# Kernel tuning notes

Hardware: AMD Instinct MI355X
Metric: run time of the kernel (lower is better)

The kernel has to match this reference:

```python
import jax, jax.numpy as jnp
import numpy as np
from math import sqrt

P = 1.0  # axis-aligned transform exponent (init arg p)
EPS = 1e-6


def setup_inputs() -> dict:
    key = jax.random.key(0)
    k1, k2, k3, k4 = jax.random.split(key, 4)
    B, L, S, H, E = 4, 2048, 2048, 8, 64
    return {
        "queries": jax.random.normal(k1, (B, L, H, E), dtype=jnp.float32),
        "keys": jax.random.normal(k2, (B, S, H, E), dtype=jnp.float32),
        "values": jax.random.normal(k3, (B, S, H, E), dtype=jnp.float32),
        "attn_mask": jnp.zeros((1, 1, 1, 1), dtype=bool),  # unused: mask_flag=False
        "directional_weights": jnp.ones((1, 1, 1, 1), dtype=jnp.float32),
        "dynamic_param": jax.random.normal(k4, (1,), dtype=jnp.float32),
    }


def _transform(x, directional_weights, dynamic_param):
    # axis_aligned_transformation: rescale by (1/std over seq dim)^p (unbiased std, like torch)
    std = jnp.std(x, axis=-2, keepdims=True, ddof=1)
    x = x * (1.0 / (std + EPS)) ** P
    # directional_reweighting then nonlinear_mapping
    x = x * directional_weights
    return jnp.tanh(x) * dynamic_param


def reference(queries, keys, values, attn_mask, directional_weights, dynamic_param):
    B, L, H, E = queries.shape
    scale = 1.0 / sqrt(E)
    qt = _transform(queries, directional_weights, dynamic_param)  # [B,L,H,E]
    kt = _transform(keys, directional_weights, dynamic_param)     # [B,S,H,E]
    scores = jnp.einsum('blhe,bshe->bhls', qt, kt)                # [B,H,L,S]
    # per-row tau = sqrt(var(scores) + eps), unbiased variance like torch.var
    tau = jnp.sqrt(jnp.var(scores, axis=-1, keepdims=True, ddof=1) + EPS)
    A = jax.nn.softmax(scale * scores / tau, axis=-1)             # [B,H,L,S]
    V = jnp.einsum('bhls,bshd->blhd', A, values)                  # [B,L,H,D]
    return V
```

## Files before the change

kernel.cpp:

```cpp
#include <hip/hip_runtime.h>
#include <math.h>

#define B_ 4
#define L_ 2048
#define S_ 2048
#define H_ 8
#define E_ 64
#define BH_ (B_*H_)
#define EPS 1e-6f
#define LOG2E 1.44269504088896340736f

typedef __attribute__((ext_vector_type(8))) short short8;
typedef __attribute__((ext_vector_type(4))) float f32x4;

__device__ __forceinline__ unsigned short f2bf(float f) {
    unsigned int u = __float_as_uint(f);
    u = (u + 0x7fffu + ((u >> 16) & 1u)) >> 16;
    return (unsigned short)u;
}

__device__ __forceinline__ float bf2f(unsigned short u) {
    return __uint_as_float(((unsigned int)u) << 16);
}

__device__ __forceinline__ float fast_tanh(float x) {
    float e = __expf(2.0f * x);
    return 1.0f - 2.0f / (e + 1.0f);
}

__device__ __forceinline__ unsigned int cvt_pk_bf16(float lo, float hi) {
    unsigned int r;
    asm("v_cvt_pk_bf16_f32 %0, %1, %2" : "=v"(r) : "v"(lo), "v"(hi));
    return r;
}
__device__ __forceinline__ float exp2_fast(float x) {
    float r;
    asm("v_exp_f32 %0, %1" : "=v"(r) : "v"(x));
    return r;
}
__device__ __forceinline__ void swap32(unsigned int &a, unsigned int &b) {
    asm("v_permlane32_swap_b32 %0, %1" : "+v"(a), "+v"(b));
}
__device__ __forceinline__ void swap16(unsigned int &a, unsigned int &b) {
    asm("v_permlane16_swap_b32 %0, %1" : "+v"(a), "+v"(b));
}

__global__ __launch_bounds__(256) void pre_kernel(
    const float* __restrict__ xq, const float* __restrict__ xk,
    const float* __restrict__ xv,
    unsigned short* __restrict__ qt, unsigned short* __restrict__ kt,
    unsigned short* __restrict__ vt,
    const float* __restrict__ dwp, const float* __restrict__ dpp)
{
    __shared__ float ls[64][65];
    int bx = blockIdx.x;
    int tid = threadIdx.x;
    if (bx < 4096) {
        const float* x = (bx < 2048) ? xq : xk;
        unsigned short* xt = (bx < 2048) ? qt : kt;
        int wv = tid >> 6, ln = tid & 63;
        int bl = (bx & 2047) * 4 + wv;
        int b = bl >> 11, l = bl & 2047;
        const float* xb = x + (size_t)bl * 512;
        float4 fa = *(const float4*)(xb + ln * 4);
        float4 fb = *(const float4*)(xb + 256 + ln * 4);
        float s0 = fa.x + fb.x, s1 = fa.y + fb.y, s2 = fa.z + fb.z, s3 = fa.w + fb.w;
        float q0 = fa.x * fa.x + fb.x * fb.x, q1 = fa.y * fa.y + fb.y * fb.y;
        float q2 = fa.z * fa.z + fb.z * fb.z, q3 = fa.w * fa.w + fb.w * fb.w;
        s0 += __shfl_xor(s0, 16); s1 += __shfl_xor(s1, 16);
        s2 += __shfl_xor(s2, 16); s3 += __shfl_xor(s3, 16);
        q0 += __shfl_xor(q0, 16); q1 += __shfl_xor(q1, 16);
        q2 += __shfl_xor(q2, 16); q3 += __shfl_xor(q3, 16);
        s0 += __shfl_xor(s0, 32); s1 += __shfl_xor(s1, 32);
        s2 += __shfl_xor(s2, 32); s3 += __shfl_xor(s3, 32);
        q0 += __shfl_xor(q0, 32); q1 += __shfl_xor(q1, 32);
        q2 += __shfl_xor(q2, 32); q3 += __shfl_xor(q3, 32);
        float dw = dwp[0], d = dpp[0];
        auto mkw = [&](float s, float q) {
            float mean = s * 0.125f;
            float var = (q - s * mean) * (1.f / 7.f);
            var = fmaxf(var, 0.f);
            return dw / (sqrtf(var) + EPS);
        };
        float w0 = mkw(s0, q0), w1 = mkw(s1, q1), w2 = mkw(s2, q2), w3 = mkw(s3, q3);
        float ta0 = fast_tanh(fa.x * w0) * d, ta1 = fast_tanh(fa.y * w1) * d;
        float ta2 = fast_tanh(fa.z * w2) * d, ta3 = fast_tanh(fa.w * w3) * d;
        float tb0 = fast_tanh(fb.x * w0) * d, tb1 = fast_tanh(fb.y * w1) * d;
        float tb2 = fast_tanh(fb.z * w2) * d, tb3 = fast_tanh(fb.w * w3) * d;
        uint2 pa, pb;
        pa.x = cvt_pk_bf16(ta0, ta1); pa.y = cvt_pk_bf16(ta2, ta3);
        pb.x = cvt_pk_bf16(tb0, tb1); pb.y = cvt_pk_bf16(tb2, tb3);
        int hh = ln >> 4, e0 = (ln & 15) * 4;
        *(uint2*)(xt + ((size_t)(b * 8 + hh) * 2048 + l) * 64 + e0) = pa;
        *(uint2*)(xt + ((size_t)(b * 8 + hh + 4) * 2048 + l) * 64 + e0) = pb;
    } else {
        int t2 = bx - 4096;
        int s0 = (t2 & 31) * 64;
        int h = (t2 >> 5) & 7, b = t2 >> 8;
        int t = tid;
#pragma unroll
        for (int i = 0; i < 4; ++i) {
            int idx = t + i * 256;
            int r = idx >> 4, c4 = (idx & 15) * 4;
            const float4 f = *(const float4*)&xv[((size_t)(b * S_ + s0 + r) * H_ + h) * E_ + c4];
            ls[r][c4] = f.x; ls[r][c4 + 1] = f.y; ls[r][c4 + 2] = f.z; ls[r][c4 + 3] = f.w;
        }
        __syncthreads();
        size_t ob = ((size_t)(b * H_ + h) * (S_ / 64) + (s0 >> 6)) * 4096;
#pragma unroll
        for (int i = 0; i < 2; ++i) {
            int ri = t + i * 256;
            int et = ri >> 7, c = (ri >> 6) & 1, quad = (ri >> 4) & 3, m = ri & 15;
            int e = et * 16 + m, sb = c * 32 + quad * 8;
            unsigned short tmp[8];
#pragma unroll
            for (int j = 0; j < 8; ++j) tmp[j] = f2bf(ls[sb + j][e]);
            *(uint4*)&vt[ob + (size_t)ri * 8] = *(uint4*)tmp;
        }
    }
}

__global__ __launch_bounds__(256) void gram_kernel(
    unsigned short* __restrict__ kt, unsigned short* __restrict__ Gb,
    float* __restrict__ ksum)
{
    __shared__ unsigned short ks[128 * 72];
    __shared__ float gs[4096];
    __shared__ float kss[64];
    int bh = blockIdx.x;
    unsigned short* base = kt + (size_t)bh * S_ * E_;
    int tid = threadIdx.x, lane = tid & 63, w = tid >> 6;
    int m = lane & 15, quad = lane >> 4;

    f32x4 acc[4][4];
#pragma unroll
    for (int i = 0; i < 4; ++i)
#pragma unroll
        for (int j = 0; j < 4; ++j) acc[i][j] = (f32x4){0.f, 0.f, 0.f, 0.f};
    float ksp[4] = {0.f, 0.f, 0.f, 0.f};

    short8 stg[4];
#pragma unroll
    for (int i = 0; i < 4; ++i)
        stg[i] = *(const short8*)(base + (size_t)(tid + i * 256) * 8);

    for (int ch = 0; ch < 16; ++ch) {
        __syncthreads();
#pragma unroll
        for (int i = 0; i < 4; ++i) {
            int u = tid + i * 256;
            *(short8*)&ks[(u >> 3) * 72 + (u & 7) * 8] = stg[i];
        }
        __syncthreads();
        if (ch < 15) {
#pragma unroll
            for (int i = 0; i < 4; ++i)
                stg[i] = *(const short8*)(base + (size_t)(ch + 1) * 8192 + (tid + i * 256) * 8);
        }
#pragma unroll
        for (int tt = 0; tt < 2; ++tt)
#pragma unroll
            for (int i = 0; i < 2; ++i) {
                int u = tid + i * 256;
                int nt = u >> 7, cc = (u >> 6) & 1, ln2 = u & 63;
                int mm = ln2 & 15, qq = ln2 >> 4;
                short8 vv = *(const short8*)&ks[(tt * 64 + nt * 16 + mm) * 72 + cc * 32 + qq * 8];
                *(uint4*)&base[(size_t)(ch * 2 + tt) * 4096 + (size_t)u * 8] = *(uint4*)&vv;
            }
        int s0 = w * 32;
        short8 af[4];
#pragma unroll
        for (int i = 0; i < 4; ++i) {
            short8 a;
#pragma unroll
            for (int kk = 0; kk < 8; ++kk) {
                unsigned short uv = ks[(s0 + quad * 8 + kk) * 72 + i * 16 + m];
                a[kk] = (short)uv;
                ksp[i] += bf2f(uv);
            }
            af[i] = a;
        }
#pragma unroll
        for (int i = 0; i < 4; ++i)
#pragma unroll
            for (int j = 0; j < 4; ++j)
                acc[i][j] = __builtin_amdgcn_mfma_f32_16x16x32_bf16(af[i], af[j], acc[i][j], 0, 0, 0);
    }
#pragma unroll
    for (int i = 0; i < 4; ++i) {
        ksp[i] += __shfl_xor(ksp[i], 16);
        ksp[i] += __shfl_xor(ksp[i], 32);
    }
    for (int w2 = 0; w2 < 4; ++w2) {
        if (w == w2) {
#pragma unroll
            for (int i = 0; i < 4; ++i)
#pragma unroll
                for (int j = 0; j < 4; ++j)
#pragma unroll
                    for (int r = 0; r < 4; ++r) {
                        int idx = (i * 16 + quad * 4 + r) * 64 + j * 16 + m;
                        if (w2 == 0) gs[idx] = acc[i][j][r]; else gs[idx] += acc[i][j][r];
                    }
            if (lane < 16) {
#pragma unroll
                for (int i = 0; i < 4; ++i) {
                    int e = i * 16 + lane;
                    if (w2 == 0) kss[e] = ksp[i]; else kss[e] += ksp[i];
                }
            }
        }
        __syncthreads();
    }
#pragma unroll
    for (int ii = 0; ii < 16; ++ii) {
        int idx = tid + ii * 256;
        Gb[(size_t)bh * 4096 + idx] = f2bf(gs[idx]);
    }
    if (tid < 64) ksum[bh * 64 + tid] = kss[tid];
}

__global__ __launch_bounds__(256, 2) void attn_kernel(
    const unsigned short* __restrict__ qt,
    const unsigned short* __restrict__ ktf,
    const unsigned short* __restrict__ vt,
    const unsigned short* __restrict__ Gb,
    const float* __restrict__ ksum,
    float* __restrict__ out)
{
    __shared__ float2 ascr_s[4 * 32];
    const int tid = threadIdx.x;
    const int lane = tid & 63;
    const int w = tid >> 6;
    const int m = lane & 15;
    const int quad = lane >> 4;
    float2* ascr = ascr_s + w * 32;

    int blk = blockIdx.x;
    int bh = (blk & 7) * 4 + ((blk >> 3) & 3);
    int l0 = (blk >> 5) * 128;
    int b = bh >> 3, h = bh & 7;

    const unsigned short* qtb = qt + (size_t)bh * L_ * E_;
    const unsigned short* kb  = ktf + (size_t)bh * S_ * E_;
    const unsigned short* vtb = vt + (size_t)bh * (S_ / 64) * 4096;

    short8 qf[2][2];
#pragma unroll
    for (int g = 0; g < 2; ++g)
#pragma unroll
        for (int c = 0; c < 2; ++c)
            qf[g][c] = *(const short8*)(qtb + (size_t)(l0 + w * 32 + g * 16 + m) * E_ + c * 32 + quad * 8);

    float al2[2], nalm2[2];
    {
        const unsigned short* gb = Gb + (size_t)bh * 4096;
        short8 gfr[4][2];
#pragma unroll
        for (int j = 0; j < 4; ++j)
#pragma unroll
            for (int c = 0; c < 2; ++c)
                gfr[j][c] = *(const short8*)(gb + (size_t)(j * 16 + m) * 64 + c * 32 + quad * 8);
        float ksl[4];
#pragma unroll
        for (int j = 0; j < 4; ++j) ksl[j] = ksum[bh * 64 + j * 16 + m];
#pragma unroll
        for (int g = 0; g < 2; ++g) {
            f32x4 accj[4];
#pragma unroll
            for (int j = 0; j < 4; ++j) {
                accj[j] = (f32x4){0.f, 0.f, 0.f, 0.f};
                accj[j] = __builtin_amdgcn_mfma_f32_16x16x32_bf16(qf[g][0], gfr[j][0], accj[j], 0, 0, 0);
                accj[j] = __builtin_amdgcn_mfma_f32_16x16x32_bf16(qf[g][1], gfr[j][1], accj[j], 0, 0, 0);
            }
            float ps[4] = {0, 0, 0, 0}, pr[4] = {0, 0, 0, 0};
#pragma unroll
            for (int r = 0; r < 4; ++r)
#pragma unroll
                for (int j = 0; j < 4; ++j) {
                    float qv = bf2f(qtb[(size_t)(l0 + w * 32 + g * 16 + quad * 4 + r) * E_ + j * 16 + m]);
                    ps[r] = fmaf(accj[j][r], qv, ps[r]);
                    pr[r] = fmaf(qv, ksl[j], pr[r]);
                }
#pragma unroll
            for (int mask = 1; mask < 16; mask <<= 1)
#pragma unroll
                for (int r = 0; r < 4; ++r) {
                    ps[r] += __shfl_xor(ps[r], mask);
                    pr[r] += __shfl_xor(pr[r], mask);
                }
            if (m == 0) {
#pragma unroll
                for (int r = 0; r < 4; ++r) {
                    float sum = pr[r];
                    float mu = sum * (1.f / S_);
                    float var = (ps[r] - sum * mu) * (1.f / (S_ - 1));
                    var = fmaxf(var, 0.f);
                    float tau = sqrtf(var + EPS);
                    float a = 0.125f / tau;
                    ascr[g * 16 + quad * 4 + r] = make_float2(a, a * mu);
                }
            }
        }
#pragma unroll
        for (int g = 0; g < 2; ++g) {
            float2 a2 = ascr[g * 16 + m];
            al2[g] = a2.x * LOG2E; nalm2[g] = -a2.y * LOG2E;
        }
    }

    f32x4 oacc[2][4];
#pragma unroll
    for (int g = 0; g < 2; ++g)
#pragma unroll
        for (int et = 0; et < 4; ++et) oacc[g][et] = (f32x4){0.f, 0.f, 0.f, 0.f};
    f32x4 asum2[2];
#pragma unroll
    for (int g = 0; g < 2; ++g) asum2[g] = (f32x4){0.f, 0.f, 0.f, 0.f};

    short8 ones;
#pragma unroll
    for (int j = 0; j < 8; ++j) ones[j] = (short)0x3F80;

#pragma unroll 2
    for (int st = 0; st < S_ / 64; ++st) {
        const unsigned short* kstb = kb + (size_t)st * 4096;
        const unsigned short* vstb = vtb + (size_t)st * 4096;
        short8 kf[4][2];
#pragma unroll
        for (int nt = 0; nt < 4; ++nt)
#pragma unroll
            for (int c = 0; c < 2; ++c)
                kf[nt][c] = *(const short8*)(kstb + (nt * 2 + c) * 512 + lane * 8);
        short8 vf[2][4];
#pragma unroll
        for (int c = 0; c < 2; ++c)
#pragma unroll
            for (int et = 0; et < 4; ++et)
                vf[c][et] = *(const short8*)(vstb + et * 1024 + c * 512 + lane * 8);

        unsigned int W[2][4][2];
#pragma unroll
        for (int nt = 0; nt < 4; ++nt)
#pragma unroll
            for (int g = 0; g < 2; ++g) {
                f32x4 acc = (f32x4){0.f, 0.f, 0.f, 0.f};
                acc = __builtin_amdgcn_mfma_f32_16x16x32_bf16(kf[nt][0], qf[g][0], acc, 0, 0, 0);
                acc = __builtin_amdgcn_mfma_f32_16x16x32_bf16(kf[nt][1], qf[g][1], acc, 0, 0, 0);
                float p0 = exp2_fast(fmaf(al2[g], acc[0], nalm2[g]));
                float p1 = exp2_fast(fmaf(al2[g], acc[1], nalm2[g]));
                float p2 = exp2_fast(fmaf(al2[g], acc[2], nalm2[g]));
                float p3 = exp2_fast(fmaf(al2[g], acc[3], nalm2[g]));
                W[g][nt][0] = cvt_pk_bf16(p0, p1);
                W[g][nt][1] = cvt_pk_bf16(p2, p3);
            }
#pragma unroll
        for (int g = 0; g < 2; ++g) {
            short8 pf[2];
#pragma unroll
            for (int c = 0; c < 2; ++c) {
                unsigned int a0 = W[g][2 * c][0], b0 = W[g][2 * c + 1][0];
                unsigned int a1 = W[g][2 * c][1], b1 = W[g][2 * c + 1][1];
                swap32(a0, b0); swap16(a0, b0);
                swap32(a1, b1); swap16(a1, b1);
                uint4 pk4;
                pk4.x = a0; pk4.y = a1; pk4.z = b0; pk4.w = b1;
                pf[c] = *(short8*)&pk4;
            }
#pragma unroll
            for (int et = 0; et < 4; ++et) {
                oacc[g][et] = __builtin_amdgcn_mfma_f32_16x16x32_bf16(pf[0], vf[0][et], oacc[g][et], 0, 0, 0);
                oacc[g][et] = __builtin_amdgcn_mfma_f32_16x16x32_bf16(pf[1], vf[1][et], oacc[g][et], 0, 0, 0);
            }
            asum2[g] = __builtin_amdgcn_mfma_f32_16x16x32_bf16(pf[0], ones, asum2[g], 0, 0, 0);
            asum2[g] = __builtin_amdgcn_mfma_f32_16x16x32_bf16(pf[1], ones, asum2[g], 0, 0, 0);
        }
    }

#pragma unroll
    for (int g = 0; g < 2; ++g)
#pragma unroll
        for (int r = 0; r < 4; ++r) {
            float rd = 1.0f / asum2[g][r];
            size_t row = (size_t)(b * L_ + l0 + w * 32 + g * 16 + quad * 4 + r);
#pragma unroll
            for (int et = 0; et < 4; ++et)
                out[(row * H_ + h) * E_ + et * 16 + m] = oacc[g][et][r] * rd;
        }
}

extern "C" void kernel_launch(void* const* d_in, const int* in_sizes, int n_in,
                              void* d_out, int out_size, void* d_ws, size_t ws_size,
                              hipStream_t stream)
{
    const float* q = (const float*)d_in[0];
    const float* k = (const float*)d_in[1];
    const float* v = (const float*)d_in[2];
    const float* dw = (const float*)d_in[4];
    const float* dp = (const float*)d_in[5];
    float* out = (float*)d_out;

    unsigned short* qt = (unsigned short*)d_ws;
    unsigned short* kt = qt + (size_t)BH_ * L_ * E_;
    unsigned short* vt = kt + (size_t)BH_ * S_ * E_;
    unsigned short* Gb = vt + (size_t)BH_ * E_ * S_;
    float* ksum = (float*)(Gb + (size_t)BH_ * 4096);

    pre_kernel<<<5120, 256, 0, stream>>>(q, k, v, qt, kt, vt, dw, dp);
    gram_kernel<<<BH_, 256, 0, stream>>>(kt, Gb, ksum);
    attn_kernel<<<512, 256, 0, stream>>>(qt, kt, vt, Gb, ksum, out);
}
```

Measured before the change: 163.4 us.

## Split Gram reduction across four blocks per head with fp32 atomics

The Gram/key-sum kernel now launches four blocks per batch-head, each covering a quarter of the sequence, instead of one block per head. Partial results are accumulated with atomicAdd into an fp32 buffer that extra blocks in the preprocessing kernel zero out first. The attention kernel converts this fp32 Gram matrix to bf16 when it loads it. This targets the low occupancy of a 32-block launch on a GPU with many CUs, at the cost of atomic traffic and a separate zeroing pass. The attention kernel also raises wave priority around its PV MFMA block.

After: 157.9 us. 3.3% less time.

```diff
diff --git a/kernel.cpp b/kernel.cpp
--- a/kernel.cpp
+++ b/kernel.cpp
@@ -49,7 +49,7 @@
     const float* __restrict__ xq, const float* __restrict__ xk,
     const float* __restrict__ xv,
     unsigned short* __restrict__ qt, unsigned short* __restrict__ kt,
-    unsigned short* __restrict__ vt,
+    unsigned short* __restrict__ vt, float* __restrict__ Gf,
     const float* __restrict__ dwp, const float* __restrict__ dpp)
 {
     __shared__ float ls[64][65];
@@ -93,7 +93,7 @@
         int hh = ln >> 4, e0 = (ln & 15) * 4;
         *(uint2*)(xt + ((size_t)(b * 8 + hh) * 2048 + l) * 64 + e0) = pa;
         *(uint2*)(xt + ((size_t)(b * 8 + hh + 4) * 2048 + l) * 64 + e0) = pb;
-    } else {
+    } else if (bx < 5120) {
         int t2 = bx - 4096;
         int s0 = (t2 & 31) * 64;
         int h = (t2 >> 5) & 7, b = t2 >> 8;
@@ -117,18 +117,21 @@
             for (int j = 0; j < 8; ++j) tmp[j] = f2bf(ls[sb + j][e]);
             *(uint4*)&vt[ob + (size_t)ri * 8] = *(uint4*)tmp;
         }
+    } else {
+        for (int i = (bx - 5120) * 256 + tid; i < 32 * 4096 + 32 * 64; i += 32 * 256)
+            Gf[i] = 0.f;
     }
 }
 
 __global__ __launch_bounds__(256) void gram_kernel(
-    unsigned short* __restrict__ kt, unsigned short* __restrict__ Gb,
+    unsigned short* __restrict__ kt, float* __restrict__ Gf,
     float* __restrict__ ksum)
 {
     __shared__ unsigned short ks[128 * 72];
     __shared__ float gs[4096];
-    __shared__ float kss[64];
-    int bh = blockIdx.x;
-    unsigned short* base = kt + (size_t)bh * S_ * E_;
+    int g2 = blockIdx.x;
+    int bh = g2 >> 2, part = g2 & 3;
+    unsigned short* base = kt + (size_t)bh * S_ * E_ + (size_t)part * 512 * E_;
     int tid = threadIdx.x, lane = tid & 63, w = tid >> 6;
     int m = lane & 15, quad = lane >> 4;
 
@@ -144,7 +147,7 @@
     for (int i = 0; i < 4; ++i)
         stg[i] = *(const short8*)(base + (size_t)(tid + i * 256) * 8);
 
-    for (int ch = 0; ch < 16; ++ch) {
+    for (int ch = 0; ch < 4; ++ch) {
         __syncthreads();
 #pragma unroll
         for (int i = 0; i < 4; ++i) {
@@ -152,7 +155,7 @@
             *(short8*)&ks[(u >> 3) * 72 + (u & 7) * 8] = stg[i];
         }
         __syncthreads();
-        if (ch < 15) {
+        if (ch < 3) {
 #pragma unroll
             for (int i = 0; i < 4; ++i)
                 stg[i] = *(const short8*)(base + (size_t)(ch + 1) * 8192 + (tid + i * 256) * 8);
@@ -191,6 +194,11 @@
         ksp[i] += __shfl_xor(ksp[i], 16);
         ksp[i] += __shfl_xor(ksp[i], 32);
     }
+    if (lane < 16) {
+#pragma unroll
+        for (int i = 0; i < 4; ++i)
+            atomicAdd(&ksum[bh * 64 + i * 16 + lane], ksp[i]);
+    }
     for (int w2 = 0; w2 < 4; ++w2) {
         if (w == w2) {
 #pragma unroll
@@ -202,29 +210,21 @@
                         int idx = (i * 16 + quad * 4 + r) * 64 + j * 16 + m;
                         if (w2 == 0) gs[idx] = acc[i][j][r]; else gs[idx] += acc[i][j][r];
                     }
-            if (lane < 16) {
-#pragma unroll
-                for (int i = 0; i < 4; ++i) {
-                    int e = i * 16 + lane;
-                    if (w2 == 0) kss[e] = ksp[i]; else kss[e] += ksp[i];
-                }
-            }
         }
         __syncthreads();
     }
 #pragma unroll
     for (int ii = 0; ii < 16; ++ii) {
         int idx = tid + ii * 256;
-        Gb[(size_t)bh * 4096 + idx] = f2bf(gs[idx]);
-    }
-    if (tid < 64) ksum[bh * 64 + tid] = kss[tid];
+        atomicAdd(&Gf[bh * 4096 + idx], gs[idx]);
+    }
 }
 
 __global__ __launch_bounds__(256, 2) void attn_kernel(
     const unsigned short* __restrict__ qt,
     const unsigned short* __restrict__ ktf,
     const unsigned short* __restrict__ vt,
-    const unsigned short* __restrict__ Gb,
+    const float* __restrict__ Gf,
     const float* __restrict__ ksum,
     float* __restrict__ out)
 {
@@ -254,13 +254,20 @@
 
     float al2[2], nalm2[2];
     {
-        const unsigned short* gb = Gb + (size_t)bh * 4096;
+        const float* gb = Gf + (size_t)bh * 4096;
         short8 gfr[4][2];
 #pragma unroll
         for (int j = 0; j < 4; ++j)
 #pragma unroll
-            for (int c = 0; c < 2; ++c)
-                gfr[j][c] = *(const short8*)(gb + (size_t)(j * 16 + m) * 64 + c * 32 + quad * 8);
+            for (int c = 0; c < 2; ++c) {
+                const float* gp = gb + (size_t)(j * 16 + m) * 64 + c * 32 + quad * 8;
+                float4 f0 = *(const float4*)gp;
+                float4 f1 = *(const float4*)(gp + 4);
+                uint4 u;
+                u.x = cvt_pk_bf16(f0.x, f0.y); u.y = cvt_pk_bf16(f0.z, f0.w);
+                u.z = cvt_pk_bf16(f1.x, f1.y); u.w = cvt_pk_bf16(f1.z, f1.w);
+                gfr[j][c] = *(short8*)&u;
+            }
         float ksl[4];
 #pragma unroll
         for (int j = 0; j < 4; ++j) ksl[j] = ksum[bh * 64 + j * 16 + m];
@@ -367,6 +374,7 @@
                 pk4.x = a0; pk4.y = a1; pk4.z = b0; pk4.w = b1;
                 pf[c] = *(short8*)&pk4;
             }
+            __builtin_amdgcn_s_setprio(1);
 #pragma unroll
             for (int et = 0; et < 4; ++et) {
                 oacc[g][et] = __builtin_amdgcn_mfma_f32_16x16x32_bf16(pf[0], vf[0][et], oacc[g][et], 0, 0, 0);
@@ -374,6 +382,7 @@
             }
             asum2[g] = __builtin_amdgcn_mfma_f32_16x16x32_bf16(pf[0], ones, asum2[g], 0, 0, 0);
             asum2[g] = __builtin_amdgcn_mfma_f32_16x16x32_bf16(pf[1], ones, asum2[g], 0, 0, 0);
+            __builtin_amdgcn_s_setprio(0);
         }
     }
 
@@ -403,10 +412,10 @@
     unsigned short* qt = (unsigned short*)d_ws;
     unsigned short* kt = qt + (size_t)BH_ * L_ * E_;
     unsigned short* vt = kt + (size_t)BH_ * S_ * E_;
-    unsigned short* Gb = vt + (size_t)BH_ * E_ * S_;
-    float* ksum = (float*)(Gb + (size_t)BH_ * 4096);
-
-    pre_kernel<<<5120, 256, 0, stream>>>(q, k, v, qt, kt, vt, dw, dp);
-    gram_kernel<<<BH_, 256, 0, stream>>>(kt, Gb, ksum);
-    attn_kernel<<<512, 256, 0, stream>>>(qt, kt, vt, Gb, ksum, out);
-}
+    float* Gf = (float*)(vt + (size_t)BH_ * E_ * S_);
+    float* ksum = Gf + (size_t)BH_ * 4096;
+
+    pre_kernel<<<5152, 256, 0, stream>>>(q, k, v, qt, kt, vt, Gf, dw, dp);
+    gram_kernel<<<128, 256, 0, stream>>>(kt, Gf, ksum);
+    attn_kernel<<<512, 256, 0, stream>>>(qt, kt, vt, Gf, ksum, out);
+}
```
